# Optimization experiments

Hardware: AMD Instinct MI355X
Metric: run time of the kernel (lower is better)

Reference implementation:

```python
import jax, jax.numpy as jnp
import numpy as np

NP_, NA_ = 100000, 50000           # paper / author node counts
E_C, E_W, E_B = 200000, 100000, 100000  # cites, writes, written_by edges
IN_DIM, OUT_DIM, H, DK = 256, 256, 8, 32
SLOPE, EPS = 0.2, 1e-5


def leaky(x):
    return jnp.where(x >= 0, x, SLOPE * x)


def seg_softmax(scores, seg, n):
    # softmax over edges grouped by destination node (DGL edge_softmax)
    m = jax.ops.segment_max(scores, seg, num_segments=n)
    e = jnp.exp(scores - m[seg])
    z = jax.ops.segment_sum(e, seg, num_segments=n)
    return e / z[seg]


def setup_inputs() -> dict:
    key = jax.random.key(0)
    k = jax.random.split(key, 14)
    s = 1.0 / np.sqrt(IN_DIM)
    return {
        "h_paper": jax.random.normal(k[0], (NP_, IN_DIM), jnp.float32),
        "h_author": jax.random.normal(k[1], (NA_, IN_DIM), jnp.float32),
        "fc_W": jax.random.normal(k[2], (OUT_DIM, IN_DIM), jnp.float32) * s,
        "fce_W": jax.random.normal(k[3], (OUT_DIM, OUT_DIM), jnp.float32) * s,
        "edge_emb": jax.random.normal(k[4], (3, OUT_DIM), jnp.float32) * 0.1,
        "attn_l": jax.random.normal(k[5], (1, H, DK), jnp.float32) * 0.1,
        "attn_r": jax.random.normal(k[6], (1, H, DK), jnp.float32) * 0.1,
        "attn_e": jax.random.normal(k[7], (1, H, DK), jnp.float32) * 0.1,
        "gamma": jnp.ones((OUT_DIM,), jnp.float32),
        "beta": jnp.zeros((OUT_DIM,), jnp.float32),
        "cites_src": jax.random.randint(k[8], (E_C,), 0, NP_),
        "cites_dst": jax.random.randint(k[9], (E_C,), 0, NP_),
        "writes_src": jax.random.randint(k[10], (E_W,), 0, NA_),
        "writes_dst": jax.random.randint(k[11], (E_W,), 0, NP_),
        "wb_src": jax.random.randint(k[12], (E_B,), 0, NP_),
        "wb_dst": jax.random.randint(k[13], (E_B,), 0, NA_),
    }


def reference(h_paper, h_author, fc_W, fce_W, edge_emb, attn_l, attn_r, attn_e,
              gamma, beta, cites_src, cites_dst, writes_src, writes_dst,
              wb_src, wb_dst):
    # fc projection (dropout = identity at eval)
    hp = (h_paper @ fc_W.T).reshape(-1, H, DK)   # [NP,H,DK]
    ha = (h_author @ fc_W.T).reshape(-1, H, DK)  # [NA,H,DK]
    # relation/edge-type embedding term: [3,H]
    ee = ((edge_emb @ fce_W.T).reshape(-1, H, DK) * attn_e).sum(-1)
    el_p = (hp * attn_l).sum(-1)  # [NP,H]
    er_p = (hp * attn_r).sum(-1)
    el_a = (ha * attn_l).sum(-1)
    er_a = (ha * attn_r).sum(-1)
    # per-edge unnormalized attention, leaky_relu(u_add_v + edge term)
    a_c = leaky(el_p[cites_src] + er_p[cites_dst] + ee[0])   # [E_C,H]
    a_w = leaky(el_a[writes_src] + er_p[writes_dst] + ee[1])  # [E_W,H]
    a_b = leaky(el_p[wb_src] + er_a[wb_dst] + ee[2])          # [E_B,H]
    # global softmax per destination node across all incoming relations
    seg_p = jnp.concatenate([cites_dst, writes_dst])
    attn_p = seg_softmax(jnp.concatenate([a_c, a_w], 0), seg_p, NP_)
    attn_a = seg_softmax(a_b, wb_dst, NA_)
    # weighted scatter-sum aggregation (u_mul_e, sum) with cross_reducer=sum
    ft_p = jnp.concatenate([hp[cites_src], ha[writes_src]], 0)  # [E,H,DK]
    t_p = jax.ops.segment_sum(ft_p * attn_p[:, :, None], seg_p,
                              num_segments=NP_).reshape(NP_, OUT_DIM)
    t_a = jax.ops.segment_sum(hp[wb_src] * attn_a[:, :, None], wb_dst,
                              num_segments=NA_).reshape(NA_, OUT_DIM)

    def ln(x):
        mu = x.mean(-1, keepdims=True)
        v = ((x - mu) ** 2).mean(-1, keepdims=True)
        return (x - mu) / jnp.sqrt(v + EPS) * gamma + beta

    out_p = ln(leaky(t_p + hp.reshape(NP_, OUT_DIM)))
    out_a = ln(leaky(t_a + ha.reshape(NA_, OUT_DIM)))
    return out_p, out_a
```

## Files before the change

### kernel.cpp

```cpp
#include <hip/hip_runtime.h>
#include <hip/hip_bf16.h>

#define NPAPER 100000
#define NAUTH  50000
#define NROWS  150000
#define EC 200000
#define EW 100000
#define EB 100000
#define ETOT 400000
#define DIM 256
#define NH 8
#define SLOPE 0.2f
#define LN_EPS 1e-5f
#define MAXD 32

#define NT 2344
#define PROJ_GRID 512
#define TPB 5

typedef unsigned short u16;
typedef __attribute__((ext_vector_type(8))) short s16x8;
typedef __attribute__((ext_vector_type(4))) float f32x4;

__device__ __forceinline__ float lrelu(float x){ return x >= 0.f ? x : SLOPE * x; }
__device__ __forceinline__ u16 f2b(float f){
  __hip_bfloat16 b = __float2bfloat16(f);
  return *reinterpret_cast<u16*>(&b);
}
__device__ __forceinline__ float b2f(u16 u){
  union { unsigned int i; float f; } v; v.i = ((unsigned int)u) << 16; return v.f;
}

__global__ void fill_i32(int* __restrict__ p, int v, int n){
  int i = blockIdx.x * blockDim.x + threadIdx.x;
  int stride = gridDim.x * blockDim.x;
  for (; i < n; i += stride) p[i] = v;
}

__global__ void prep_kernel(const float* __restrict__ fcW, const float* __restrict__ fceW,
                            const float* __restrict__ eEmb, const float* __restrict__ attn_e,
                            u16* __restrict__ Wb, float* __restrict__ eew)
{
  const int blk = blockIdx.x, tid = threadIdx.x;
  if (blk < 64){
    int i = blk * 256 + tid;
    float4 v = reinterpret_cast<const float4*>(fcW)[i];
    ushort4 o; o.x = f2b(v.x); o.y = f2b(v.y); o.z = f2b(v.z); o.w = f2b(v.w);
    reinterpret_cast<ushort4*>(Wb)[i] = o;
  } else {
    int b = blk - 64;
    int rel = b / 16, cg = b % 16;
    int wid = tid >> 6, l = tid & 63;
    int h = cg >> 1;
    float4 e4 = *reinterpret_cast<const float4*>(eEmb + rel * DIM + l * 4);
    float acc = 0.f;
    #pragma unroll
    for (int cc = 0; cc < 4; cc++){
      int c = cg * 16 + wid * 4 + cc;
      float4 w4 = *reinterpret_cast<const float4*>(fceW + (size_t)c * DIM + l * 4);
      float d = w4.x*e4.x + w4.y*e4.y + w4.z*e4.z + w4.w*e4.w;
      acc += d * attn_e[c];
    }
    #pragma unroll
    for (int m = 32; m > 0; m >>= 1) acc += __shfl_xor(acc, m, 64);
    if (l == 0) atomicAdd(&eew[rel * NH + h], acc);
  }
}

__global__ __launch_bounds__(512) void proj_mfma(
    const float* __restrict__ hP, const float* __restrict__ hA,
    const u16* __restrict__ Wb, u16* __restrict__ out)
{
  const int tid = threadIdx.x;
  const int l = tid & 63, wid = tid >> 6;
  const int lrow = l & 15, g = l >> 4;
  __shared__ u16 xs[2][64 * 256];

  const int t0 = blockIdx.x * TPB;
  if (t0 >= NT) return;
  const int nt = min(TPB, NT - t0);

  s16x8 bW0[8], bW1[8];
  {
    const u16* b0 = Wb + (size_t)(32 * wid + lrow) * DIM + g * 8;
    const u16* b1 = b0 + 16 * DIM;
    #pragma unroll
    for (int k = 0; k < 8; k++){
      bW0[k] = *reinterpret_cast<const s16x8*>(b0 + k * 32);
      bW1[k] = *reinterpret_cast<const s16x8*>(b1 + k * 32);
    }
  }

  float4 v[8];
  #pragma unroll
  for (int it = 0; it < 8; it++){
    int i = tid + it * 512;
    int row = i >> 6, c4 = (i & 63) << 2;
    int gr = t0 * 64 + row; gr = gr < NROWS ? gr : NROWS - 1;
    const float* base = (gr < NPAPER) ? hP + (size_t)gr * DIM + c4
                                      : hA + (size_t)(gr - NPAPER) * DIM + c4;
    v[it] = *reinterpret_cast<const float4*>(base);
  }
  #pragma unroll
  for (int it = 0; it < 8; it++){
    int i = tid + it * 512;
    int row = i >> 6, c4 = (i & 63) << 2;
    ushort4 o; o.x = f2b(v[it].x); o.y = f2b(v[it].y); o.z = f2b(v[it].z); o.w = f2b(v[it].w);
    int byte = (row * 256 + c4) * 2;
    byte ^= (row & 7) << 4;
    *reinterpret_cast<ushort4*>((char*)&xs[0][0] + byte) = o;
  }
  __syncthreads();

  for (int i = 0; i < nt; i++){
    const int cur = i & 1;
    const bool more = (i + 1 < nt);
    const int r0 = (t0 + i) * 64;
    if (more){
      #pragma unroll
      for (int it = 0; it < 8; it++){
        int ii = tid + it * 512;
        int row = ii >> 6, c4 = (ii & 63) << 2;
        int gr = r0 + 64 + row; gr = gr < NROWS ? gr : NROWS - 1;
        const float* base = (gr < NPAPER) ? hP + (size_t)gr * DIM + c4
                                          : hA + (size_t)(gr - NPAPER) * DIM + c4;
        v[it] = *reinterpret_cast<const float4*>(base);
      }
    }
    f32x4 acc[4][2];
    #pragma unroll
    for (int mi = 0; mi < 4; mi++){
      acc[mi][0] = (f32x4){0.f,0.f,0.f,0.f};
      acc[mi][1] = (f32x4){0.f,0.f,0.f,0.f};
    }
    #pragma unroll
    for (int kk = 0; kk < 8; kk++){
      s16x8 aF[4];
      #pragma unroll
      for (int mi = 0; mi < 4; mi++){
        int row = mi * 16 + lrow;
        int byte = (row * 256 + kk * 32 + g * 8) * 2;
        byte ^= (row & 7) << 4;
        aF[mi] = *reinterpret_cast<const s16x8*>((const char*)&xs[cur][0] + byte);
      }
      #pragma unroll
      for (int mi = 0; mi < 4; mi++){
        acc[mi][0] = __builtin_amdgcn_mfma_f32_16x16x32_bf16(bW0[kk], aF[mi], acc[mi][0], 0, 0, 0);
        acc[mi][1] = __builtin_amdgcn_mfma_f32_16x16x32_bf16(bW1[kk], aF[mi], acc[mi][1], 0, 0, 0);
      }
    }
    #pragma unroll
    for (int mi = 0; mi < 4; mi++){
      int grow = r0 + mi * 16 + lrow;
      if (grow < NROWS){
        #pragma unroll
        for (int ni = 0; ni < 2; ni++){
          int col = 32 * wid + ni * 16 + g * 4;
          ushort4 o;
          o.x = f2b(acc[mi][ni][0]); o.y = f2b(acc[mi][ni][1]);
          o.z = f2b(acc[mi][ni][2]); o.w = f2b(acc[mi][ni][3]);
          *reinterpret_cast<ushort4*>(out + (size_t)grow * DIM + col) = o;
        }
      }
    }
    if (more){
      #pragma unroll
      for (int it = 0; it < 8; it++){
        int ii = tid + it * 512;
        int row = ii >> 6, c4 = (ii & 63) << 2;
        ushort4 o; o.x = f2b(v[it].x); o.y = f2b(v[it].y); o.z = f2b(v[it].z); o.w = f2b(v[it].w);
        int byte = (row * 256 + c4) * 2;
        byte ^= (row & 7) << 4;
        *reinterpret_cast<ushort4*>((char*)&xs[1 - cur][0] + byte) = o;
      }
    }
    __syncthreads();
  }
}

__global__ __launch_bounds__(256) void elr_kernel(const u16* __restrict__ hprojb,
    const float* __restrict__ attn_l, const float* __restrict__ attn_r,
    float* __restrict__ el, float* __restrict__ er)
{
  const int wid = threadIdx.x >> 6, l = threadIdx.x & 63;
  const int row = blockIdx.x * 4 + wid;
  if (row >= NROWS) return;
  ushort4 u = *reinterpret_cast<const ushort4*>(hprojb + (size_t)row * DIM + l * 4);
  float v0 = b2f(u.x), v1 = b2f(u.y), v2 = b2f(u.z), v3 = b2f(u.w);
  float4 al = *reinterpret_cast<const float4*>(attn_l + l * 4);
  float4 ar = *reinterpret_cast<const float4*>(attn_r + l * 4);
  float sl = v0*al.x + v1*al.y + v2*al.z + v3*al.w;
  float sr = v0*ar.x + v1*ar.y + v2*ar.z + v3*ar.w;
  #pragma unroll
  for (int m = 1; m < 8; m <<= 1){
    sl += __shfl_xor(sl, m, 64);
    sr += __shfl_xor(sr, m, 64);
  }
  if ((l & 7) == 0){
    int h = l >> 3;
    el[(size_t)row*NH+h] = sl;
    er[(size_t)row*NH+h] = sr;
  }
}

__global__ void scatter_direct(const int* __restrict__ c_src, const int* __restrict__ c_dst,
                               const int* __restrict__ w_src, const int* __restrict__ w_dst,
                               const int* __restrict__ b_src, const int* __restrict__ b_dst,
                               int* __restrict__ cursor, int* __restrict__ eidx){
  int i = blockIdx.x * blockDim.x + threadIdx.x;
  int gd, pk;
  if (i < EC)           { gd = c_dst[i];                pk = c_src[i]; }
  else if (i < EC + EW) { gd = w_dst[i - EC];           pk = (w_src[i - EC] + NPAPER) | (1 << 20); }
  else if (i < ETOT)    { gd = NPAPER + b_dst[i - EC - EW]; pk = b_src[i - EC - EW] | (2 << 20); }
  else return;
  int pos = atomicAdd(&cursor[gd], 1);
  if (pos < MAXD) eidx[(size_t)gd * MAXD + pos] = pk;
}

template<int K>
__device__ __forceinline__ void proc_edges(
    const int* __restrict__ erow, int base, int cnt,
    const float* __restrict__ el, float er_h,
    float ee0, float ee1, float ee2,
    const u16* __restrict__ hprojb, int l, int h,
    float& ax, float& ay, float& az, float& aw, float& zl)
{
  int pk[K]; float w[K]; ushort4 u[K];
  #pragma unroll
  for (int j = 0; j < K; j++)
    pk[j] = erow[base + (j < cnt ? j : 0)];
  #pragma unroll
  for (int j = 0; j < K; j++){
    int gs = pk[j] & 0xFFFFF, rl = pk[j] >> 20;
    u[j] = *reinterpret_cast<const ushort4*>(hprojb + (size_t)gs * DIM + l * 4);
    float sc = el[(size_t)gs * NH + h] + er_h + (rl == 0 ? ee0 : (rl == 1 ? ee1 : ee2));
    w[j] = (j < cnt) ? __expf(lrelu(sc)) : 0.f;
  }
  #pragma unroll
  for (int j = 0; j < K; j++){
    zl += w[j];
    ax += w[j] * b2f(u[j].x); ay += w[j] * b2f(u[j].y);
    az += w[j] * b2f(u[j].z); aw += w[j] * b2f(u[j].w);
  }
}

__global__ __launch_bounds__(256) void agg_ln_kernel(
    const int* __restrict__ counts, const int* __restrict__ eidx,
    const u16* __restrict__ hprojb,
    const float* __restrict__ el, const float* __restrict__ er,
    const float* __restrict__ eew, const float* __restrict__ gamma,
    const float* __restrict__ beta, float* __restrict__ out)
{
  const int wid = threadIdx.x >> 6, l = threadIdx.x & 63;
  const int r = blockIdx.x * 4 + wid;
  if (r >= NROWS) return;
  const int h = l >> 3;
  const float er_h = er[(size_t)r * NH + h];
  const float ee0 = eew[h], ee1 = eew[NH + h], ee2 = eew[2*NH + h];
  const int deg = min(counts[r], MAXD);
  const int* erow = eidx + (size_t)r * MAXD;

  float ax = 0.f, ay = 0.f, az = 0.f, aw = 0.f, zl = 0.f;
  int base = 0;
  while (deg - base >= 8){
    proc_edges<8>(erow, base, 8, el, er_h, ee0, ee1, ee2, hprojb, l, h, ax, ay, az, aw, zl);
    base += 8;
  }
  int rem = deg - base;
  if (rem > 4)      proc_edges<8>(erow, base, rem, el, er_h, ee0, ee1, ee2, hprojb, l, h, ax, ay, az, aw, zl);
  else if (rem > 2) proc_edges<4>(erow, base, rem, el, er_h, ee0, ee1, ee2, hprojb, l, h, ax, ay, az, aw, zl);
  else if (rem > 0) proc_edges<2>(erow, base, rem, el, er_h, ee0, ee1, ee2, hprojb, l, h, ax, ay, az, aw, zl);

  float iz = (deg > 0) ? 1.f / zl : 0.f;
  ushort4 hr = *reinterpret_cast<const ushort4*>(hprojb + (size_t)r * DIM + l * 4);
  float x0 = lrelu(ax * iz + b2f(hr.x));
  float x1 = lrelu(ay * iz + b2f(hr.y));
  float x2 = lrelu(az * iz + b2f(hr.z));
  float x3 = lrelu(aw * iz + b2f(hr.w));
  float s = x0 + x1 + x2 + x3;
  float q = x0*x0 + x1*x1 + x2*x2 + x3*x3;
  #pragma unroll
  for (int m = 32; m > 0; m >>= 1){
    s += __shfl_xor(s, m, 64);
    q += __shfl_xor(q, m, 64);
  }
  float mu  = s * (1.f / DIM);
  float var = q * (1.f / DIM) - mu * mu;
  float inv = rsqrtf(var + LN_EPS);
  float4 g  = *reinterpret_cast<const float4*>(gamma + l * 4);
  float4 bt = *reinterpret_cast<const float4*>(beta + l * 4);
  float4 o;
  o.x = (x0 - mu) * inv * g.x + bt.x;
  o.y = (x1 - mu) * inv * g.y + bt.y;
  o.z = (x2 - mu) * inv * g.z + bt.z;
  o.w = (x3 - mu) * inv * g.w + bt.w;
  *reinterpret_cast<float4*>(out + (size_t)r * DIM + l * 4) = o;
}

extern "C" void kernel_launch(void* const* d_in, const int* in_sizes, int n_in,
                              void* d_out, int out_size, void* d_ws, size_t ws_size,
                              hipStream_t stream)
{
  const float* hP     = (const float*)d_in[0];
  const float* hA     = (const float*)d_in[1];
  const float* fcW    = (const float*)d_in[2];
  const float* fceW   = (const float*)d_in[3];
  const float* eEmb   = (const float*)d_in[4];
  const float* attn_l = (const float*)d_in[5];
  const float* attn_r = (const float*)d_in[6];
  const float* attn_e = (const float*)d_in[7];
  const float* gamma  = (const float*)d_in[8];
  const float* beta   = (const float*)d_in[9];
  const int* c_src  = (const int*)d_in[10];
  const int* c_dst  = (const int*)d_in[11];
  const int* w_src  = (const int*)d_in[12];
  const int* w_dst  = (const int*)d_in[13];
  const int* b_src  = (const int*)d_in[14];
  const int* b_dst  = (const int*)d_in[15];

  u16*   hprojb = (u16*)d_ws;
  float* el    = (float*)(hprojb + (size_t)NROWS * DIM);
  float* er    = el    + (size_t)NROWS * NH;
  float* eew   = er    + (size_t)NROWS * NH;
  int*   cursor= (int*)(eew + 32);
  int*   eidx  = cursor + NROWS;
  u16*   Wb    = (u16*)(eidx + (size_t)NROWS * MAXD);

  const int TB = 256;

  fill_i32<<<256, TB, 0, stream>>>((int*)eew, 0, 32 + NROWS);
  scatter_direct<<<(ETOT + TB - 1) / TB, TB, 0, stream>>>(c_src, c_dst, w_src, w_dst,
                                                          b_src, b_dst, cursor, eidx);

  prep_kernel<<<112, TB, 0, stream>>>(fcW, fceW, eEmb, attn_e, Wb, eew);
  proj_mfma<<<PROJ_GRID, 512, 0, stream>>>(hP, hA, Wb, hprojb);
  elr_kernel<<<(NROWS + 3) / 4, TB, 0, stream>>>(hprojb, attn_l, attn_r, el, er);

  agg_ln_kernel<<<NROWS / 4, TB, 0, stream>>>(cursor, eidx, hprojb,
                                              el, er, eew, gamma, beta,
                                              (float*)d_out);
}
```

Baseline: 190.4 us.

## Merge projection, edge scatter and relation prep into one kernel; recompute el/er in aggregation

The separate prep, projection and scatter launches become one heterogeneous mega-kernel whose blocks are split by role. Projection blocks convert fc_W to bf16 in registers instead of reading a pre-converted copy, and the relation-embedding term is computed per block without atomics. The elr kernel is removed: er is computed from the destination's own projected row, and el from each neighbour's row already loaded for aggregation, using 8-lane shuffle reductions. This saves launches and the el/er round trip to memory, at the cost of extra ALU and shuffle work per edge in the aggregation loop and uneven block types sharing one grid.

Result: slower. 206.0 us (+8.2%).

```diff
diff --git a/kernel.cpp b/kernel.cpp
--- a/kernel.cpp
+++ b/kernel.cpp
@@ -15,8 +15,9 @@
 #define MAXD 32
 
 #define NT 2344
-#define PROJ_GRID 512
+#define PROJ_BLKS 512
 #define TPB 5
+#define SCAT_BLKS 782
 
 typedef unsigned short u16;
 typedef __attribute__((ext_vector_type(8))) short s16x8;
@@ -37,192 +38,163 @@
   for (; i < n; i += stride) p[i] = v;
 }
 
-__global__ void prep_kernel(const float* __restrict__ fcW, const float* __restrict__ fceW,
-                            const float* __restrict__ eEmb, const float* __restrict__ attn_e,
-                            u16* __restrict__ Wb, float* __restrict__ eew)
+__global__ __launch_bounds__(512) void mega_kernel(
+    const float* __restrict__ hP, const float* __restrict__ hA,
+    const float* __restrict__ fcW, const float* __restrict__ fceW,
+    const float* __restrict__ eEmb, const float* __restrict__ attn_e,
+    const int* __restrict__ c_src, const int* __restrict__ c_dst,
+    const int* __restrict__ w_src, const int* __restrict__ w_dst,
+    const int* __restrict__ b_src, const int* __restrict__ b_dst,
+    u16* __restrict__ out, float* __restrict__ eew,
+    int* __restrict__ cursor, int* __restrict__ eidx)
 {
+  __shared__ u16 xs[2][64 * 256];
   const int blk = blockIdx.x, tid = threadIdx.x;
-  if (blk < 64){
-    int i = blk * 256 + tid;
-    float4 v = reinterpret_cast<const float4*>(fcW)[i];
-    ushort4 o; o.x = f2b(v.x); o.y = f2b(v.y); o.z = f2b(v.z); o.w = f2b(v.w);
-    reinterpret_cast<ushort4*>(Wb)[i] = o;
-  } else {
-    int b = blk - 64;
-    int rel = b / 16, cg = b % 16;
-    int wid = tid >> 6, l = tid & 63;
-    int h = cg >> 1;
-    float4 e4 = *reinterpret_cast<const float4*>(eEmb + rel * DIM + l * 4);
-    float acc = 0.f;
+
+  if (blk < PROJ_BLKS){
+    const int l = tid & 63, wid = tid >> 6;
+    const int lrow = l & 15, g = l >> 4;
+    const int t0 = blk * TPB;
+    if (t0 >= NT) return;
+    const int nt = min(TPB, NT - t0);
+
+    s16x8 bW0[8], bW1[8];
+    {
+      const float* b0 = fcW + (size_t)(32 * wid + lrow) * DIM + g * 8;
+      const float* b1 = b0 + 16 * DIM;
+      #pragma unroll
+      for (int k = 0; k < 8; k++){
+        float4 f0 = *reinterpret_cast<const float4*>(b0 + k * 32);
+        float4 f1 = *reinterpret_cast<const float4*>(b0 + k * 32 + 4);
+        float4 f2 = *reinterpret_cast<const float4*>(b1 + k * 32);
+        float4 f3 = *reinterpret_cast<const float4*>(b1 + k * 32 + 4);
+        s16x8 t0v, t1v;
+        t0v[0]=(short)f2b(f0.x); t0v[1]=(short)f2b(f0.y); t0v[2]=(short)f2b(f0.z); t0v[3]=(short)f2b(f0.w);
+        t0v[4]=(short)f2b(f1.x); t0v[5]=(short)f2b(f1.y); t0v[6]=(short)f2b(f1.z); t0v[7]=(short)f2b(f1.w);
+        t1v[0]=(short)f2b(f2.x); t1v[1]=(short)f2b(f2.y); t1v[2]=(short)f2b(f2.z); t1v[3]=(short)f2b(f2.w);
+        t1v[4]=(short)f2b(f3.x); t1v[5]=(short)f2b(f3.y); t1v[6]=(short)f2b(f3.z); t1v[7]=(short)f2b(f3.w);
+        bW0[k] = t0v; bW1[k] = t1v;
+      }
+    }
+
+    float4 v[8];
     #pragma unroll
-    for (int cc = 0; cc < 4; cc++){
-      int c = cg * 16 + wid * 4 + cc;
-      float4 w4 = *reinterpret_cast<const float4*>(fceW + (size_t)c * DIM + l * 4);
-      float d = w4.x*e4.x + w4.y*e4.y + w4.z*e4.z + w4.w*e4.w;
-      acc += d * attn_e[c];
+    for (int it = 0; it < 8; it++){
+      int i = tid + it * 512;
+      int row = i >> 6, c4 = (i & 63) << 2;
+      int gr = t0 * 64 + row; gr = gr < NROWS ? gr : NROWS - 1;
+      const float* base = (gr < NPAPER) ? hP + (size_t)gr * DIM + c4
+                                        : hA + (size_t)(gr - NPAPER) * DIM + c4;
+      v[it] = *reinterpret_cast<const float4*>(base);
     }
     #pragma unroll
-    for (int m = 32; m > 0; m >>= 1) acc += __shfl_xor(acc, m, 64);
-    if (l == 0) atomicAdd(&eew[rel * NH + h], acc);
-  }
-}
-
-__global__ __launch_bounds__(512) void proj_mfma(
-    const float* __restrict__ hP, const float* __restrict__ hA,
-    const u16* __restrict__ Wb, u16* __restrict__ out)
-{
-  const int tid = threadIdx.x;
-  const int l = tid & 63, wid = tid >> 6;
-  const int lrow = l & 15, g = l >> 4;
-  __shared__ u16 xs[2][64 * 256];
-
-  const int t0 = blockIdx.x * TPB;
-  if (t0 >= NT) return;
-  const int nt = min(TPB, NT - t0);
-
-  s16x8 bW0[8], bW1[8];
-  {
-    const u16* b0 = Wb + (size_t)(32 * wid + lrow) * DIM + g * 8;
-    const u16* b1 = b0 + 16 * DIM;
-    #pragma unroll
-    for (int k = 0; k < 8; k++){
-      bW0[k] = *reinterpret_cast<const s16x8*>(b0 + k * 32);
-      bW1[k] = *reinterpret_cast<const s16x8*>(b1 + k * 32);
-    }
-  }
-
-  float4 v[8];
-  #pragma unroll
-  for (int it = 0; it < 8; it++){
-    int i = tid + it * 512;
-    int row = i >> 6, c4 = (i & 63) << 2;
-    int gr = t0 * 64 + row; gr = gr < NROWS ? gr : NROWS - 1;
-    const float* base = (gr < NPAPER) ? hP + (size_t)gr * DIM + c4
-                                      : hA + (size_t)(gr - NPAPER) * DIM + c4;
-    v[it] = *reinterpret_cast<const float4*>(base);
-  }
-  #pragma unroll
-  for (int it = 0; it < 8; it++){
-    int i = tid + it * 512;
-    int row = i >> 6, c4 = (i & 63) << 2;
-    ushort4 o; o.x = f2b(v[it].x); o.y = f2b(v[it].y); o.z = f2b(v[it].z); o.w = f2b(v[it].w);
-    int byte = (row * 256 + c4) * 2;
-    byte ^= (row & 7) << 4;
-    *reinterpret_cast<ushort4*>((char*)&xs[0][0] + byte) = o;
-  }
-  __syncthreads();
-
-  for (int i = 0; i < nt; i++){
-    const int cur = i & 1;
-    const bool more = (i + 1 < nt);
-    const int r0 = (t0 + i) * 64;
-    if (more){
-      #pragma unroll
-      for (int it = 0; it < 8; it++){
-        int ii = tid + it * 512;
-        int row = ii >> 6, c4 = (ii & 63) << 2;
-        int gr = r0 + 64 + row; gr = gr < NROWS ? gr : NROWS - 1;
-        const float* base = (gr < NPAPER) ? hP + (size_t)gr * DIM + c4
-                                          : hA + (size_t)(gr - NPAPER) * DIM + c4;
-        v[it] = *reinterpret_cast<const float4*>(base);
-      }
-    }
-    f32x4 acc[4][2];
-    #pragma unroll
-    for (int mi = 0; mi < 4; mi++){
-      acc[mi][0] = (f32x4){0.f,0.f,0.f,0.f};
-      acc[mi][1] = (f32x4){0.f,0.f,0.f,0.f};
-    }
-    #pragma unroll
-    for (int kk = 0; kk < 8; kk++){
-      s16x8 aF[4];
+    for (int it = 0; it < 8; it++){
+      int i = tid + it * 512;
+      int row = i >> 6, c4 = (i & 63) << 2;
+      ushort4 o; o.x = f2b(v[it].x); o.y = f2b(v[it].y); o.z = f2b(v[it].z); o.w = f2b(v[it].w);
+      int byte = (row * 256 + c4) * 2;
+      byte ^= (row & 7) << 4;
+      *reinterpret_cast<ushort4*>((char*)&xs[0][0] + byte) = o;
+    }
+    __syncthreads();
+
+    for (int i = 0; i < nt; i++){
+      const int cur = i & 1;
+      const bool more = (i + 1 < nt);
+      const int r0 = (t0 + i) * 64;
+      if (more){
+        #pragma unroll
+        for (int it = 0; it < 8; it++){
+          int ii = tid + it * 512;
+          int row = ii >> 6, c4 = (ii & 63) << 2;
+          int gr = r0 + 64 + row; gr = gr < NROWS ? gr : NROWS - 1;
+          const float* base = (gr < NPAPER) ? hP + (size_t)gr * DIM + c4
+                                            : hA + (size_t)(gr - NPAPER) * DIM + c4;
+          v[it] = *reinterpret_cast<const float4*>(base);
+        }
+      }
+      f32x4 acc[4][2];
       #pragma unroll
       for (int mi = 0; mi < 4; mi++){
-        int row = mi * 16 + lrow;
-        int byte = (row * 256 + kk * 32 + g * 8) * 2;
-        byte ^= (row & 7) << 4;
-        aF[mi] = *reinterpret_cast<const s16x8*>((const char*)&xs[cur][0] + byte);
+        acc[mi][0] = (f32x4){0.f,0.f,0.f,0.f};
+        acc[mi][1] = (f32x4){0.f,0.f,0.f,0.f};
+      }
+      #pragma unroll
+      for (int kk = 0; kk < 8; kk++){
+        s16x8 aF[4];
+        #pragma unroll
+        for (int mi = 0; mi < 4; mi++){
+          int row = mi * 16 + lrow;
+          int byte = (row * 256 + kk * 32 + g * 8) * 2;
+          byte ^= (row & 7) << 4;
+          aF[mi] = *reinterpret_cast<const s16x8*>((const char*)&xs[cur][0] + byte);
+        }
+        #pragma unroll
+        for (int mi = 0; mi < 4; mi++){
+          acc[mi][0] = __builtin_amdgcn_mfma_f32_16x16x32_bf16(bW0[kk], aF[mi], acc[mi][0], 0, 0, 0);
+          acc[mi][1] = __builtin_amdgcn_mfma_f32_16x16x32_bf16(bW1[kk], aF[mi], acc[mi][1], 0, 0, 0);
+        }
       }
       #pragma unroll
       for (int mi = 0; mi < 4; mi++){
-        acc[mi][0] = __builtin_amdgcn_mfma_f32_16x16x32_bf16(bW0[kk], aF[mi], acc[mi][0], 0, 0, 0);
-        acc[mi][1] = __builtin_amdgcn_mfma_f32_16x16x32_bf16(bW1[kk], aF[mi], acc[mi][1], 0, 0, 0);
-      }
-    }
+        int grow = r0 + mi * 16 + lrow;
+        if (grow < NROWS){
+          #pragma unroll
+          for (int ni = 0; ni < 2; ni++){
+            int col = 32 * wid + ni * 16 + g * 4;
+            ushort4 o;
+            o.x = f2b(acc[mi][ni][0]); o.y = f2b(acc[mi][ni][1]);
+            o.z = f2b(acc[mi][ni][2]); o.w = f2b(acc[mi][ni][3]);
+            *reinterpret_cast<ushort4*>(out + (size_t)grow * DIM + col) = o;
+          }
+        }
+      }
+      if (more){
+        #pragma unroll
+        for (int it = 0; it < 8; it++){
+          int ii = tid + it * 512;
+          int row = ii >> 6, c4 = (ii & 63) << 2;
+          ushort4 o; o.x = f2b(v[it].x); o.y = f2b(v[it].y); o.z = f2b(v[it].z); o.w = f2b(v[it].w);
+          int byte = (row * 256 + c4) * 2;
+          byte ^= (row & 7) << 4;
+          *reinterpret_cast<ushort4*>((char*)&xs[1 - cur][0] + byte) = o;
+        }
+      }
+      __syncthreads();
+    }
+  } else if (blk < PROJ_BLKS + SCAT_BLKS){
+    int i = (blk - PROJ_BLKS) * 512 + tid;
+    int gd, pk;
+    if (i < EC)           { gd = c_dst[i];                pk = c_src[i]; }
+    else if (i < EC + EW) { gd = w_dst[i - EC];           pk = (w_src[i - EC] + NPAPER) | (1 << 20); }
+    else if (i < ETOT)    { gd = NPAPER + b_dst[i - EC - EW]; pk = b_src[i - EC - EW] | (2 << 20); }
+    else return;
+    int pos = atomicAdd(&cursor[gd], 1);
+    if (pos < MAXD) eidx[(size_t)gd * MAXD + pos] = pk;
+  } else {
+    if (tid >= 256) return;
+    const int rel = blk - PROJ_BLKS - SCAT_BLKS;
+    const int c = tid;
+    float acc = 0.f;
+    const float4* er4 = reinterpret_cast<const float4*>(eEmb + rel * DIM);
+    const float4* wr4 = reinterpret_cast<const float4*>(fceW + (size_t)c * DIM);
+    for (int k = 0; k < 64; k++){
+      float4 e4 = er4[k], w4 = wr4[k];
+      acc += w4.x*e4.x + w4.y*e4.y + w4.z*e4.z + w4.w*e4.w;
+    }
+    acc *= attn_e[c];
     #pragma unroll
-    for (int mi = 0; mi < 4; mi++){
-      int grow = r0 + mi * 16 + lrow;
-      if (grow < NROWS){
-        #pragma unroll
-        for (int ni = 0; ni < 2; ni++){
-          int col = 32 * wid + ni * 16 + g * 4;
-          ushort4 o;
-          o.x = f2b(acc[mi][ni][0]); o.y = f2b(acc[mi][ni][1]);
-          o.z = f2b(acc[mi][ni][2]); o.w = f2b(acc[mi][ni][3]);
-          *reinterpret_cast<ushort4*>(out + (size_t)grow * DIM + col) = o;
-        }
-      }
-    }
-    if (more){
-      #pragma unroll
-      for (int it = 0; it < 8; it++){
-        int ii = tid + it * 512;
-        int row = ii >> 6, c4 = (ii & 63) << 2;
-        ushort4 o; o.x = f2b(v[it].x); o.y = f2b(v[it].y); o.z = f2b(v[it].z); o.w = f2b(v[it].w);
-        int byte = (row * 256 + c4) * 2;
-        byte ^= (row & 7) << 4;
-        *reinterpret_cast<ushort4*>((char*)&xs[1 - cur][0] + byte) = o;
-      }
-    }
-    __syncthreads();
-  }
-}
-
-__global__ __launch_bounds__(256) void elr_kernel(const u16* __restrict__ hprojb,
-    const float* __restrict__ attn_l, const float* __restrict__ attn_r,
-    float* __restrict__ el, float* __restrict__ er)
-{
-  const int wid = threadIdx.x >> 6, l = threadIdx.x & 63;
-  const int row = blockIdx.x * 4 + wid;
-  if (row >= NROWS) return;
-  ushort4 u = *reinterpret_cast<const ushort4*>(hprojb + (size_t)row * DIM + l * 4);
-  float v0 = b2f(u.x), v1 = b2f(u.y), v2 = b2f(u.z), v3 = b2f(u.w);
-  float4 al = *reinterpret_cast<const float4*>(attn_l + l * 4);
-  float4 ar = *reinterpret_cast<const float4*>(attn_r + l * 4);
-  float sl = v0*al.x + v1*al.y + v2*al.z + v3*al.w;
-  float sr = v0*ar.x + v1*ar.y + v2*ar.z + v3*ar.w;
-  #pragma unroll
-  for (int m = 1; m < 8; m <<= 1){
-    sl += __shfl_xor(sl, m, 64);
-    sr += __shfl_xor(sr, m, 64);
-  }
-  if ((l & 7) == 0){
-    int h = l >> 3;
-    el[(size_t)row*NH+h] = sl;
-    er[(size_t)row*NH+h] = sr;
-  }
-}
-
-__global__ void scatter_direct(const int* __restrict__ c_src, const int* __restrict__ c_dst,
-                               const int* __restrict__ w_src, const int* __restrict__ w_dst,
-                               const int* __restrict__ b_src, const int* __restrict__ b_dst,
-                               int* __restrict__ cursor, int* __restrict__ eidx){
-  int i = blockIdx.x * blockDim.x + threadIdx.x;
-  int gd, pk;
-  if (i < EC)           { gd = c_dst[i];                pk = c_src[i]; }
-  else if (i < EC + EW) { gd = w_dst[i - EC];           pk = (w_src[i - EC] + NPAPER) | (1 << 20); }
-  else if (i < ETOT)    { gd = NPAPER + b_dst[i - EC - EW]; pk = b_src[i - EC - EW] | (2 << 20); }
-  else return;
-  int pos = atomicAdd(&cursor[gd], 1);
-  if (pos < MAXD) eidx[(size_t)gd * MAXD + pos] = pk;
+    for (int m = 1; m < 32; m <<= 1) acc += __shfl_xor(acc, m, 64);
+    if ((c & 31) == 0) eew[rel * NH + (c >> 5)] = acc;
+  }
 }
 
 template<int K>
 __device__ __forceinline__ void proc_edges(
     const int* __restrict__ erow, int base, int cnt,
-    const float* __restrict__ el, float er_h,
+    float er_h, float4 al4,
     float ee0, float ee1, float ee2,
-    const u16* __restrict__ hprojb, int l, int h,
+    const u16* __restrict__ hprojb, int l,
     float& ax, float& ay, float& az, float& aw, float& zl)
 {
   int pk[K]; float w[K]; ushort4 u[K];
@@ -231,9 +203,18 @@
     pk[j] = erow[base + (j < cnt ? j : 0)];
   #pragma unroll
   for (int j = 0; j < K; j++){
-    int gs = pk[j] & 0xFFFFF, rl = pk[j] >> 20;
+    int gs = pk[j] & 0xFFFFF;
     u[j] = *reinterpret_cast<const ushort4*>(hprojb + (size_t)gs * DIM + l * 4);
-    float sc = el[(size_t)gs * NH + h] + er_h + (rl == 0 ? ee0 : (rl == 1 ? ee1 : ee2));
+  }
+  #pragma unroll
+  for (int j = 0; j < K; j++){
+    int rl = pk[j] >> 20;
+    float elp = b2f(u[j].x)*al4.x + b2f(u[j].y)*al4.y
+              + b2f(u[j].z)*al4.z + b2f(u[j].w)*al4.w;
+    elp += __shfl_xor(elp, 1, 64);
+    elp += __shfl_xor(elp, 2, 64);
+    elp += __shfl_xor(elp, 4, 64);
+    float sc = elp + er_h + (rl == 0 ? ee0 : (rl == 1 ? ee1 : ee2));
     w[j] = (j < cnt) ? __expf(lrelu(sc)) : 0.f;
   }
   #pragma unroll
@@ -247,7 +228,7 @@
 __global__ __launch_bounds__(256) void agg_ln_kernel(
     const int* __restrict__ counts, const int* __restrict__ eidx,
     const u16* __restrict__ hprojb,
-    const float* __restrict__ el, const float* __restrict__ er,
+    const float* __restrict__ attn_l, const float* __restrict__ attn_r,
     const float* __restrict__ eew, const float* __restrict__ gamma,
     const float* __restrict__ beta, float* __restrict__ out)
 {
@@ -255,28 +236,35 @@
   const int r = blockIdx.x * 4 + wid;
   if (r >= NROWS) return;
   const int h = l >> 3;
-  const float er_h = er[(size_t)r * NH + h];
   const float ee0 = eew[h], ee1 = eew[NH + h], ee2 = eew[2*NH + h];
+  const float4 al4 = *reinterpret_cast<const float4*>(attn_l + l * 4);
+  const float4 ar4 = *reinterpret_cast<const float4*>(attn_r + l * 4);
   const int deg = min(counts[r], MAXD);
   const int* erow = eidx + (size_t)r * MAXD;
+
+  ushort4 hr = *reinterpret_cast<const ushort4*>(hprojb + (size_t)r * DIM + l * 4);
+  float h0 = b2f(hr.x), h1 = b2f(hr.y), h2 = b2f(hr.z), h3 = b2f(hr.w);
+  float er_h = h0*ar4.x + h1*ar4.y + h2*ar4.z + h3*ar4.w;
+  er_h += __shfl_xor(er_h, 1, 64);
+  er_h += __shfl_xor(er_h, 2, 64);
+  er_h += __shfl_xor(er_h, 4, 64);
 
   float ax = 0.f, ay = 0.f, az = 0.f, aw = 0.f, zl = 0.f;
   int base = 0;
   while (deg - base >= 8){
-    proc_edges<8>(erow, base, 8, el, er_h, ee0, ee1, ee2, hprojb, l, h, ax, ay, az, aw, zl);
+    proc_edges<8>(erow, base, 8, er_h, al4, ee0, ee1, ee2, hprojb, l, ax, ay, az, aw, zl);
     base += 8;
   }
   int rem = deg - base;
-  if (rem > 4)      proc_edges<8>(erow, base, rem, el, er_h, ee0, ee1, ee2, hprojb, l, h, ax, ay, az, aw, zl);
-  else if (rem > 2) proc_edges<4>(erow, base, rem, el, er_h, ee0, ee1, ee2, hprojb, l, h, ax, ay, az, aw, zl);
-  else if (rem > 0) proc_edges<2>(erow, base, rem, el, er_h, ee0, ee1, ee2, hprojb, l, h, ax, ay, az, aw, zl);
+  if (rem > 4)      proc_edges<8>(erow, base, rem, er_h, al4, ee0, ee1, ee2, hprojb, l, ax, ay, az, aw, zl);
+  else if (rem > 2) proc_edges<4>(erow, base, rem, er_h, al4, ee0, ee1, ee2, hprojb, l, ax, ay, az, aw, zl);
+  else if (rem > 0) proc_edges<2>(erow, base, rem, er_h, al4, ee0, ee1, ee2, hprojb, l, ax, ay, az, aw, zl);
 
   float iz = (deg > 0) ? 1.f / zl : 0.f;
-  ushort4 hr = *reinterpret_cast<const ushort4*>(hprojb + (size_t)r * DIM + l * 4);
-  float x0 = lrelu(ax * iz + b2f(hr.x));
-  float x1 = lrelu(ay * iz + b2f(hr.y));
-  float x2 = lrelu(az * iz + b2f(hr.z));
-  float x3 = lrelu(aw * iz + b2f(hr.w));
+  float x0 = lrelu(ax * iz + h0);
+  float x1 = lrelu(ay * iz + h1);
+  float x2 = lrelu(az * iz + h2);
+  float x3 = lrelu(aw * iz + h3);
   float s = x0 + x1 + x2 + x3;
   float q = x0*x0 + x1*x1 + x2*x2 + x3*x3;
   #pragma unroll
@@ -319,24 +307,16 @@
   const int* b_dst  = (const int*)d_in[15];
 
   u16*   hprojb = (u16*)d_ws;
-  float* el    = (float*)(hprojb + (size_t)NROWS * DIM);
-  float* er    = el    + (size_t)NROWS * NH;
-  float* eew   = er    + (size_t)NROWS * NH;
+  float* eew   = (float*)(hprojb + (size_t)NROWS * DIM);
   int*   cursor= (int*)(eew + 32);
   int*   eidx  = cursor + NROWS;
-  u16*   Wb    = (u16*)(eidx + (size_t)NROWS * MAXD);
-
-  const int TB = 256;
-
-  fill_i32<<<256, TB, 0, stream>>>((int*)eew, 0, 32 + NROWS);
-  scatter_direct<<<(ETOT + TB - 1) / TB, TB, 0, stream>>>(c_src, c_dst, w_src, w_dst,
-                                                          b_src, b_dst, cursor, eidx);
-
-  prep_kernel<<<112, TB, 0, stream>>>(fcW, fceW, eEmb, attn_e, Wb, eew);
-  proj_mfma<<<PROJ_GRID, 512, 0, stream>>>(hP, hA, Wb, hprojb);
-  elr_kernel<<<(NROWS + 3) / 4, TB, 0, stream>>>(hprojb, attn_l, attn_r, el, er);
-
-  agg_ln_kernel<<<NROWS / 4, TB, 0, stream>>>(cursor, eidx, hprojb,
-                                              el, er, eew, gamma, beta,
-                                              (float*)d_out);
-}
+
+  fill_i32<<<256, 256, 0, stream>>>(cursor, 0, NROWS);
+  mega_kernel<<<PROJ_BLKS + SCAT_BLKS + 3, 512, 0, stream>>>(
+      hP, hA, fcW, fceW, eEmb, attn_e,
+      c_src, c_dst, w_src, w_dst, b_src, b_dst,
+      hprojb, eew, cursor, eidx);
+  agg_ln_kernel<<<NROWS / 4, 256, 0, stream>>>(cursor, eidx, hprojb,
+                                               attn_l, attn_r, eew, gamma, beta,
+                                               (float*)d_out);
+}
```

## Stage projection input via direct global-to-LDS loads with 32-row tiles

Applied to the files above, without the earlier changes.

The projection GEMM now loads fp32 input rows straight into shared memory with global_load_lds, instead of going through registers, converting to bf16 and storing to LDS. It uses a rotated layout to avoid bank conflicts and waits on explicit vmcnt counters for double buffering. The tile shrinks from 64 to 32 rows, with 10 tiles per block. The bf16 conversion moves to after the LDS read, which adds ALU work per MFMA operand, and the hand-written waitcnt and barrier sequencing is fragile.

New measurement: 190.8 us. No clear change (+0.2%).

```diff
diff --git a/kernel.cpp b/kernel.cpp
--- a/kernel.cpp
+++ b/kernel.cpp
@@ -14,9 +14,12 @@
 #define LN_EPS 1e-5f
 #define MAXD 32
 
-#define NT 2344
-#define PROJ_GRID 512
-#define TPB 5
+#define NT32 4688
+#define TPB2 10
+#define PROJ_GRID2 469
+
+#define AS1 __attribute__((address_space(1)))
+#define AS3 __attribute__((address_space(3)))
 
 typedef unsigned short u16;
 typedef __attribute__((ext_vector_type(8))) short s16x8;
@@ -74,11 +77,11 @@
   const int tid = threadIdx.x;
   const int l = tid & 63, wid = tid >> 6;
   const int lrow = l & 15, g = l >> 4;
-  __shared__ u16 xs[2][64 * 256];
-
-  const int t0 = blockIdx.x * TPB;
-  if (t0 >= NT) return;
-  const int nt = min(TPB, NT - t0);
+  __shared__ u16 xs[2][16384];
+
+  const int t0 = blockIdx.x * TPB2;
+  if (t0 >= NT32) return;
+  const int nt = min(TPB2, NT32 - t0);
 
   s16x8 bW0[8], bW1[8];
   {
@@ -91,90 +94,82 @@
     }
   }
 
-  float4 v[8];
-  #pragma unroll
-  for (int it = 0; it < 8; it++){
-    int i = tid + it * 512;
-    int row = i >> 6, c4 = (i & 63) << 2;
-    int gr = t0 * 64 + row; gr = gr < NROWS ? gr : NROWS - 1;
-    const float* base = (gr < NPAPER) ? hP + (size_t)gr * DIM + c4
-                                      : hA + (size_t)(gr - NPAPER) * DIM + c4;
-    v[it] = *reinterpret_cast<const float4*>(base);
-  }
-  #pragma unroll
-  for (int it = 0; it < 8; it++){
-    int i = tid + it * 512;
-    int row = i >> 6, c4 = (i & 63) << 2;
-    ushort4 o; o.x = f2b(v[it].x); o.y = f2b(v[it].y); o.z = f2b(v[it].z); o.w = f2b(v[it].w);
-    int byte = (row * 256 + c4) * 2;
-    byte ^= (row & 7) << 4;
-    *reinterpret_cast<ushort4*>((char*)&xs[0][0] + byte) = o;
-  }
-  __syncthreads();
+  auto stage = [&](int t, int buf){
+    #pragma unroll
+    for (int j = 0; j < 4; j++){
+      int rb = wid * 4 + j;
+      int gr = t * 32 + rb;
+      gr = gr < NROWS ? gr : NROWS - 1;
+      const float* rowp = (gr < NPAPER) ? hP + (size_t)gr * DIM
+                                        : hA + (size_t)(gr - NPAPER) * DIM;
+      const float* src = rowp + (((l + rb) & 63) << 2);
+      __builtin_amdgcn_global_load_lds((const AS1 void*)src,
+                                       (AS3 void*)&xs[buf][rb << 9], 16, 0, 0);
+    }
+  };
+
+  stage(t0, 0);
 
   for (int i = 0; i < nt; i++){
     const int cur = i & 1;
     const bool more = (i + 1 < nt);
-    const int r0 = (t0 + i) * 64;
-    if (more){
+    if (more) stage(t0 + i + 1, 1 - cur);
+
+    if (i == 0 || !more) { asm volatile("s_waitcnt vmcnt(4)" ::: "memory"); }
+    else                 { asm volatile("s_waitcnt vmcnt(8)" ::: "memory"); }
+    __builtin_amdgcn_s_barrier();
+    __builtin_amdgcn_sched_barrier(0);
+
+    f32x4 acc[2][2];
+    acc[0][0] = (f32x4){0.f,0.f,0.f,0.f}; acc[0][1] = (f32x4){0.f,0.f,0.f,0.f};
+    acc[1][0] = (f32x4){0.f,0.f,0.f,0.f}; acc[1][1] = (f32x4){0.f,0.f,0.f,0.f};
+
+    const char* lbase = (const char*)&xs[cur][0];
+    #pragma unroll
+    for (int kk = 0; kk < 8; kk++){
+      s16x8 aF[2];
       #pragma unroll
-      for (int it = 0; it < 8; it++){
-        int ii = tid + it * 512;
-        int row = ii >> 6, c4 = (ii & 63) << 2;
-        int gr = r0 + 64 + row; gr = gr < NROWS ? gr : NROWS - 1;
-        const float* base = (gr < NPAPER) ? hP + (size_t)gr * DIM + c4
-                                          : hA + (size_t)(gr - NPAPER) * DIM + c4;
-        v[it] = *reinterpret_cast<const float4*>(base);
-      }
-    }
-    f32x4 acc[4][2];
-    #pragma unroll
-    for (int mi = 0; mi < 4; mi++){
-      acc[mi][0] = (f32x4){0.f,0.f,0.f,0.f};
-      acc[mi][1] = (f32x4){0.f,0.f,0.f,0.f};
-    }
-    #pragma unroll
-    for (int kk = 0; kk < 8; kk++){
-      s16x8 aF[4];
-      #pragma unroll
-      for (int mi = 0; mi < 4; mi++){
-        int row = mi * 16 + lrow;
-        int byte = (row * 256 + kk * 32 + g * 8) * 2;
-        byte ^= (row & 7) << 4;
-        aF[mi] = *reinterpret_cast<const s16x8*>((const char*)&xs[cur][0] + byte);
+      for (int mi = 0; mi < 2; mi++){
+        int r = mi * 16 + lrow;
+        int c0 = kk * 8 + g * 2;
+        const char* rowb = lbase + (r << 10);
+        f32x4 a0 = *reinterpret_cast<const f32x4*>(rowb + ((((c0    ) - r) & 63) << 4));
+        f32x4 a1 = *reinterpret_cast<const f32x4*>(rowb + ((((c0 + 1) - r) & 63) << 4));
+        s16x8 af;
+        af[0] = (short)f2b(a0[0]); af[1] = (short)f2b(a0[1]);
+        af[2] = (short)f2b(a0[2]); af[3] = (short)f2b(a0[3]);
+        af[4] = (short)f2b(a1[0]); af[5] = (short)f2b(a1[1]);
+        af[6] = (short)f2b(a1[2]); af[7] = (short)f2b(a1[3]);
+        aF[mi] = af;
       }
       #pragma unroll
-      for (int mi = 0; mi < 4; mi++){
+      for (int mi = 0; mi < 2; mi++){
         acc[mi][0] = __builtin_amdgcn_mfma_f32_16x16x32_bf16(bW0[kk], aF[mi], acc[mi][0], 0, 0, 0);
         acc[mi][1] = __builtin_amdgcn_mfma_f32_16x16x32_bf16(bW1[kk], aF[mi], acc[mi][1], 0, 0, 0);
       }
     }
-    #pragma unroll
-    for (int mi = 0; mi < 4; mi++){
-      int grow = r0 + mi * 16 + lrow;
-      if (grow < NROWS){
-        #pragma unroll
-        for (int ni = 0; ni < 2; ni++){
-          int col = 32 * wid + ni * 16 + g * 4;
-          ushort4 o;
-          o.x = f2b(acc[mi][ni][0]); o.y = f2b(acc[mi][ni][1]);
-          o.z = f2b(acc[mi][ni][2]); o.w = f2b(acc[mi][ni][3]);
-          *reinterpret_cast<ushort4*>(out + (size_t)grow * DIM + col) = o;
+
+    {
+      int r0 = (t0 + i) * 32;
+      #pragma unroll
+      for (int mi = 0; mi < 2; mi++){
+        int grow = r0 + mi * 16 + lrow;
+        if (grow < NROWS){
+          #pragma unroll
+          for (int ni = 0; ni < 2; ni++){
+            int col = 32 * wid + ni * 16 + g * 4;
+            ushort4 o;
+            o.x = f2b(acc[mi][ni][0]); o.y = f2b(acc[mi][ni][1]);
+            o.z = f2b(acc[mi][ni][2]); o.w = f2b(acc[mi][ni][3]);
+            *reinterpret_cast<ushort4*>(out + (size_t)grow * DIM + col) = o;
+          }
         }
       }
     }
-    if (more){
-      #pragma unroll
-      for (int it = 0; it < 8; it++){
-        int ii = tid + it * 512;
-        int row = ii >> 6, c4 = (ii & 63) << 2;
-        ushort4 o; o.x = f2b(v[it].x); o.y = f2b(v[it].y); o.z = f2b(v[it].z); o.w = f2b(v[it].w);
-        int byte = (row * 256 + c4) * 2;
-        byte ^= (row & 7) << 4;
-        *reinterpret_cast<ushort4*>((char*)&xs[1 - cur][0] + byte) = o;
-      }
-    }
-    __syncthreads();
+
+    asm volatile("s_waitcnt lgkmcnt(0)" ::: "memory");
+    __builtin_amdgcn_s_barrier();
+    __builtin_amdgcn_sched_barrier(0);
   }
 }
 
@@ -333,7 +328,7 @@
                                                           b_src, b_dst, cursor, eidx);
 
   prep_kernel<<<112, TB, 0, stream>>>(fcW, fceW, eEmb, attn_e, Wb, eew);
-  proj_mfma<<<PROJ_GRID, 512, 0, stream>>>(hP, hA, Wb, hprojb);
+  proj_mfma<<<PROJ_GRID2, 512, 0, stream>>>(hP, hA, Wb, hprojb);
   elr_kernel<<<(NROWS + 3) / 4, TB, 0, stream>>>(hprojb, attn_l, attn_r, el, er);
 
   agg_ln_kernel<<<NROWS / 4, TB, 0, stream>>>(cursor, eidx, hprojb,
```
